# Performance work log

Measured on AMD Instinct MI355X. Metric: run time of the kernel, lower is better.

## Reference

```python
import jax, jax.numpy as jnp
import numpy as np


def setup_inputs() -> dict:
    key = jax.random.key(0)
    k1, k2, k3 = jax.random.split(key, 3)
    VOCAB, DIM = 1_000_000, 64
    N_IDS = 819_200       # ~16384 segments * avg 50 ids each
    NUM_SEGMENTS = 16_384
    params = jax.random.normal(k1, (VOCAB, DIM), dtype=jnp.float32)
    ids = jax.random.randint(k2, (N_IDS,), 0, VOCAB, dtype=jnp.int64)
    segment_ids = jnp.sort(jax.random.randint(k3, (N_IDS,), 0, NUM_SEGMENTS, dtype=jnp.int64))
    return {"params": params, "ids": ids, "segment_ids": segment_ids, "num_segments": NUM_SEGMENTS}


def reference(params, ids, segment_ids, num_segments):
    # tf.nn.embedding_lookup_sparse(params, sp_ids, None, combiner='sum')
    # == segment-sum of gathered embedding rows over the sparse row (segment) ids.
    gathered = params[ids]  # [N_IDS, DIM]
    out = jax.ops.segment_sum(gathered, segment_ids, num_segments=num_segments)
    return out.astype(params.dtype)
```

## Files before the change

kernel.cpp:

```cpp
#include <hip/hip_runtime.h>

#define DIM 64

__device__ __forceinline__ void f4acc(float4& a, const float4& v) {
    a.x += v.x; a.y += v.y; a.z += v.z; a.w += v.w;
}

__global__ void seg_offsets_kernel(const int* __restrict__ seg, int* __restrict__ offsets,
                                   int n_ids, int num_segments)
{
    int i = blockIdx.x * blockDim.x + threadIdx.x;
    if (i >= n_ids) return;
    int cur  = seg[i];
    int prev = (i == 0) ? -1 : seg[i - 1];
    for (int s = prev + 1; s <= cur; ++s) offsets[s] = i;
    if (i == n_ids - 1) {
        for (int s = cur + 1; s <= num_segments; ++s) offsets[s] = n_ids;
    }
}

template <bool USE_OFFSETS>
__global__ __launch_bounds__(256) void emb_seg_sum_kernel(
    const float* __restrict__ params,
    const int*   __restrict__ ids,
    const int*   __restrict__ seg_or_off,
    float*       __restrict__ out,
    int n_ids, int num_segments)
{
    const int gtid = blockIdx.x * blockDim.x + threadIdx.x;
    const int wseg = gtid >> 6;
    const int lane = threadIdx.x & 63;
    if (wseg >= num_segments) return;

    int start, end;
    if (USE_OFFSETS) {
        start = seg_or_off[wseg];
        end   = seg_or_off[wseg + 1];
    } else {
        int lo = 0, hi = n_ids;
        while (lo < hi) {
            int mid = (lo + hi) >> 1;
            if (seg_or_off[mid] < wseg) lo = mid + 1; else hi = mid;
        }
        start = lo;
        hi = n_ids;
        while (lo < hi) {
            int mid = (lo + hi) >> 1;
            if (seg_or_off[mid] <= wseg) lo = mid + 1; else hi = mid;
        }
        end = lo;
    }

    const int sub  = lane >> 4;
    const int col4 = lane & 15;
    const float* __restrict__ pcol = params + col4 * 4;

    float4 a0 = {0,0,0,0}, a1 = {0,0,0,0}, a2 = {0,0,0,0}, a3 = {0,0,0,0};

    for (int base = start; base < end; base += 64) {
        const int cnt = min(64, end - base);
        int myid = 0;
        if (base + lane < end) myid = ids[base + lane];

        int j = 0;
        for (; j + 16 <= cnt; j += 16) {
            const int i0 = __shfl(myid, j      + sub);
            const int i1 = __shfl(myid, j + 4  + sub);
            const int i2 = __shfl(myid, j + 8  + sub);
            const int i3 = __shfl(myid, j + 12 + sub);
            const float4 v0 = *(const float4*)(pcol + (size_t)i0 * DIM);
            const float4 v1 = *(const float4*)(pcol + (size_t)i1 * DIM);
            const float4 v2 = *(const float4*)(pcol + (size_t)i2 * DIM);
            const float4 v3 = *(const float4*)(pcol + (size_t)i3 * DIM);
            f4acc(a0, v0); f4acc(a1, v1); f4acc(a2, v2); f4acc(a3, v3);
        }
        for (; j + 4 <= cnt; j += 4) {
            const int i0 = __shfl(myid, j + sub);
            f4acc(a1, *(const float4*)(pcol + (size_t)i0 * DIM));
        }
        if (j < cnt) {
            const int r  = j + sub;
            const int i0 = __shfl(myid, (r < cnt) ? r : j);
            if (r < cnt) {
                f4acc(a2, *(const float4*)(pcol + (size_t)i0 * DIM));
            }
        }
    }

    f4acc(a0, a1); f4acc(a2, a3); f4acc(a0, a2);

    a0.x += __shfl_xor(a0.x, 16); a0.y += __shfl_xor(a0.y, 16);
    a0.z += __shfl_xor(a0.z, 16); a0.w += __shfl_xor(a0.w, 16);
    a0.x += __shfl_xor(a0.x, 32); a0.y += __shfl_xor(a0.y, 32);
    a0.z += __shfl_xor(a0.z, 32); a0.w += __shfl_xor(a0.w, 32);

    if (lane < 16) {
        *(float4*)(out + (size_t)wseg * DIM + col4 * 4) = a0;
    }
}

extern "C" void kernel_launch(void* const* d_in, const int* in_sizes, int n_in,
                              void* d_out, int out_size, void* d_ws, size_t ws_size,
                              hipStream_t stream)
{
    const float* params = (const float*)d_in[0];
    const int*   ids    = (const int*)d_in[1];
    const int*   seg    = (const int*)d_in[2];
    float*       out    = (float*)d_out;

    const int n_ids        = in_sizes[1];
    const int num_segments = out_size / DIM;

    const int threads = 256;
    const int waves_per_block = threads / 64;
    const int grid = (num_segments + waves_per_block - 1) / waves_per_block;

    const size_t off_bytes = (size_t)(num_segments + 1) * sizeof(int);
    if (ws_size >= off_bytes) {
        int* offsets = (int*)d_ws;
        seg_offsets_kernel<<<(n_ids + 255) / 256, 256, 0, stream>>>(
            seg, offsets, n_ids, num_segments);
        emb_seg_sum_kernel<true><<<grid, threads, 0, stream>>>(
            params, ids, offsets, out, n_ids, num_segments);
    } else {
        emb_seg_sum_kernel<false><<<grid, threads, 0, stream>>>(
            params, ids, seg, out, n_ids, num_segments);
    }
}
```

Before: 42.23 us.

## Replace offsets pre-pass with galloping search from uniform segment position guess

Removes the separate segment-offsets kernel launch and finds each segment's bounds inside the main kernel. Each wave guesses its start position from the uniform distribution of segment ids, then gallops outward and binary-searches. This saves one kernel launch and a pass over the segment array, at the cost of a few dependent global loads per wave before the gather starts.

```diff
diff --git a/kernel.cpp b/kernel.cpp
--- a/kernel.cpp
+++ b/kernel.cpp
@@ -6,24 +6,44 @@
     a.x += v.x; a.y += v.y; a.z += v.z; a.w += v.w;
 }
 
-__global__ void seg_offsets_kernel(const int* __restrict__ seg, int* __restrict__ offsets,
-                                   int n_ids, int num_segments)
+__device__ __forceinline__ int lower_bound_gallop(
+    const int* __restrict__ seg, int n, int key, int guess)
 {
-    int i = blockIdx.x * blockDim.x + threadIdx.x;
-    if (i >= n_ids) return;
-    int cur  = seg[i];
-    int prev = (i == 0) ? -1 : seg[i - 1];
-    for (int s = prev + 1; s <= cur; ++s) offsets[s] = i;
-    if (i == n_ids - 1) {
-        for (int s = cur + 1; s <= num_segments; ++s) offsets[s] = n_ids;
+    if (guess < 0) guess = 0;
+    if (guess > n) guess = n;
+    int lo, hi;
+    if (guess >= n || seg[guess] >= key) {
+        hi = guess;
+        int step = 256;
+        lo = 0;
+        for (;;) {
+            int probe = hi - step;
+            if (probe <= 0) { lo = 0; break; }
+            if (seg[probe] >= key) { hi = probe; step <<= 1; }
+            else { lo = probe + 1; break; }
+        }
+    } else {
+        lo = guess + 1;
+        hi = n;
+        int step = 256;
+        for (;;) {
+            int probe = lo + step;
+            if (probe >= n) { hi = n; break; }
+            if (seg[probe] < key) { lo = probe + 1; step <<= 1; }
+            else { hi = probe; break; }
+        }
     }
+    while (lo < hi) {
+        int mid = (lo + hi) >> 1;
+        if (seg[mid] < key) lo = mid + 1; else hi = mid;
+    }
+    return lo;
 }
 
-template <bool USE_OFFSETS>
 __global__ __launch_bounds__(256) void emb_seg_sum_kernel(
     const float* __restrict__ params,
     const int*   __restrict__ ids,
-    const int*   __restrict__ seg_or_off,
+    const int*   __restrict__ seg,
     float*       __restrict__ out,
     int n_ids, int num_segments)
 {
@@ -32,24 +52,10 @@
     const int lane = threadIdx.x & 63;
     if (wseg >= num_segments) return;
 
-    int start, end;
-    if (USE_OFFSETS) {
-        start = seg_or_off[wseg];
-        end   = seg_or_off[wseg + 1];
-    } else {
-        int lo = 0, hi = n_ids;
-        while (lo < hi) {
-            int mid = (lo + hi) >> 1;
-            if (seg_or_off[mid] < wseg) lo = mid + 1; else hi = mid;
-        }
-        start = lo;
-        hi = n_ids;
-        while (lo < hi) {
-            int mid = (lo + hi) >> 1;
-            if (seg_or_off[mid] <= wseg) lo = mid + 1; else hi = mid;
-        }
-        end = lo;
-    }
+    const int avg = n_ids / num_segments;
+    const int guess = (int)(((long long)wseg * n_ids) / num_segments);
+    const int start = lower_bound_gallop(seg, n_ids, wseg, guess);
+    const int end   = lower_bound_gallop(seg, n_ids, wseg + 1, start + avg);
 
     const int sub  = lane >> 4;
     const int col4 = lane & 15;
@@ -115,15 +121,6 @@
     const int waves_per_block = threads / 64;
     const int grid = (num_segments + waves_per_block - 1) / waves_per_block;
 
-    const size_t off_bytes = (size_t)(num_segments + 1) * sizeof(int);
-    if (ws_size >= off_bytes) {
-        int* offsets = (int*)d_ws;
-        seg_offsets_kernel<<<(n_ids + 255) / 256, 256, 0, stream>>>(
-            seg, offsets, n_ids, num_segments);
-        emb_seg_sum_kernel<true><<<grid, threads, 0, stream>>>(
-            params, ids, offsets, out, n_ids, num_segments);
-    } else {
-        emb_seg_sum_kernel<false><<<grid, threads, 0, stream>>>(
-            params, ids, seg, out, n_ids, num_segments);
-    }
+    emb_seg_sum_kernel<<<grid, threads, 0, stream>>>(
+        params, ids, seg, out, n_ids, num_segments);
 }
```

Result: slower. 45.19 us (+7.0%).
